# Performance work log

Measured on AMD Instinct MI355X. Metric: run time of the kernel, lower is better.

## Reference

```python
import jax, jax.numpy as jnp
import numpy as np

T, N, D, E = 4, 50000, 32, 800000
V_TH = 1.0      # v_threshold
ALPHA = 4.0     # surrogate-gradient sharpness


def setup_inputs() -> dict:
    key = jax.random.key(0)
    k1, k2, k3, k4 = jax.random.split(key, 4)
    s_seq = jax.random.normal(k1, (T, N, D), dtype=jnp.float32) * 0.5
    z_seq = jax.random.normal(k2, (N, D), dtype=jnp.float32) * 0.5
    edge_index = jax.random.randint(k3, (2, E), 0, N, dtype=jnp.int64)
    # GCNConv weight (bias=False), Glorot-ish scale
    W = jax.random.normal(k4, (D, D), dtype=jnp.float32) / np.sqrt(D).astype(np.float32)
    return {"s_seq": s_seq, "z_seq": z_seq, "W": W, "edge_index": edge_index}


def _gcn_conv(x, W, edge_index, n_nodes):
    """PyG GCNConv with add_self_loops=True, normalize=True, bias=False.
    x: [T,N,D]; returns [T,N,D]."""
    src, dst = edge_index[0], edge_index[1]
    ones = jnp.ones(src.shape[0], dtype=x.dtype)
    deg = jax.ops.segment_sum(ones, dst, num_segments=n_nodes) + 1.0  # +1 self loop
    dinv = jax.lax.rsqrt(deg)                                        # [N]
    xw = jnp.einsum('tnd,df->tnf', x, W)                             # dense transform
    norm = dinv[src] * dinv[dst]                                     # [E]
    msgs = xw[:, src, :] * norm[None, :, None]                       # [T,E,D] gather
    agg = jax.vmap(lambda m: jax.ops.segment_sum(m, dst, num_segments=n_nodes))(msgs)
    # self-loop contribution with norm dinv[i]^2
    return agg + xw * (dinv * dinv)[None, :, None]


def _spike(v):
    # Heaviside spike with surrogate (sigmoid) gradient, straight-through.
    s = (v >= V_TH).astype(v.dtype)
    sg = jax.nn.sigmoid(ALPHA * (v - V_TH))
    return s + sg - jax.lax.stop_gradient(sg)


def reference(s_seq, z_seq, W, edge_index):
    n_nodes = s_seq.shape[1]
    x_seq = _gcn_conv(s_seq, W, edge_index, n_nodes)   # [T,N,D]  (dropout p=0.0 is identity)
    y_seq = x_seq.mean(0)                              # temporal mean [N,D]
    # Riemannian IF node: integrate-and-fire over time with soft reset;
    # latent state z drifts by the temporal mean (Euclidean proxy for expmap).
    def step(v, x_t):
        v = v + x_t
        o = _spike(v)
        v = v - o * V_TH
        return v, o
    v0 = jnp.zeros_like(z_seq)
    _, o_seq = jax.lax.scan(step, v0, x_seq)           # [T,N,D]
    z_new = z_seq + y_seq
    return o_seq, z_new
```

## Files before the change

### kernel.cpp

```cpp
#include <hip/hip_runtime.h>
#include <hip/hip_fp16.h>

#define TSTEPS 4
#define DIM 32
#define BINW_SHIFT 8
#define NB 256
#define HB 128
#define GROWS 128
#define SP_CH 2048
#define PAD_PER_BIN 772

__device__ __forceinline__ float4 ldx4h(const __half* p) {
    uint2 u = *(const uint2*)p;
    __half2 h0 = *(__half2*)&u.x;
    __half2 h1 = *(__half2*)&u.y;
    float2 a = __half22float2(h0);
    float2 b = __half22float2(h1);
    return make_float4(a.x, a.y, b.x, b.y);
}

__global__ __launch_bounds__(256) void hist_kernel(
    const int* __restrict__ ei, int* __restrict__ ghistPB, int* __restrict__ cursor,
    int E, int hch) {
    __shared__ int lh[NB];
    int tid = threadIdx.x;
    lh[tid] = 0;
    __syncthreads();
    int beg = blockIdx.x * hch;
    int end = min(beg + hch, E);
    for (int e = beg + tid; e < end; e += 256)
        atomicAdd(&lh[ei[E + e] >> BINW_SHIFT], 1);
    __syncthreads();
    ghistPB[blockIdx.x * NB + tid] = lh[tid];
    if (blockIdx.x == 0) cursor[tid] = 0;
}

__global__ __launch_bounds__(256) void splitgemm_kernel(
    const int* __restrict__ ei, const int* __restrict__ ghistPB,
    int* __restrict__ cursor, unsigned int* __restrict__ esorted,
    int* __restrict__ binScan,
    const float* __restrict__ s, const float* __restrict__ W,
    __half* __restrict__ xwp, int E, int rows, int N, int nchunks) {
    __shared__ __align__(16) char smem[22528];
    int tid = threadIdx.x;

    if ((int)blockIdx.x >= nchunks) {
        float4 (*sW4)[8] = (float4 (*)[8])smem;
        float  (*sS)[36] = (float (*)[36])(smem + 4096);
        int row = tid >> 3;
        int cg  = tid & 7;
        sW4[row][cg] = ((const float4*)W)[tid];
        int rowBase = ((int)blockIdx.x - nchunks) * GROWS;
#pragma unroll
        for (int j = 0; j < 4; j++) {
            int r = rowBase + row + j * 32;
            float4 sv = (r < rows) ? ((const float4*)s)[(size_t)r * 8 + cg]
                                   : make_float4(0.f, 0.f, 0.f, 0.f);
            *(float4*)&sS[row + j * 32][cg * 4] = sv;
        }
        __syncthreads();
        float4 a0 = make_float4(0.f, 0.f, 0.f, 0.f);
        float4 a1 = a0, a2 = a0, a3 = a0;
#pragma unroll
        for (int k = 0; k < 32; k++) {
            float4 wv = sW4[k][cg];
            float s0 = sS[row][k];
            float s1 = sS[row + 32][k];
            float s2 = sS[row + 64][k];
            float s3 = sS[row + 96][k];
            a0.x += s0 * wv.x; a0.y += s0 * wv.y; a0.z += s0 * wv.z; a0.w += s0 * wv.w;
            a1.x += s1 * wv.x; a1.y += s1 * wv.y; a1.z += s1 * wv.z; a1.w += s1 * wv.w;
            a2.x += s2 * wv.x; a2.y += s2 * wv.y; a2.z += s2 * wv.z; a2.w += s2 * wv.w;
            a3.x += s3 * wv.x; a3.y += s3 * wv.y; a3.z += s3 * wv.z; a3.w += s3 * wv.w;
        }
        float4 accs[4] = {a0, a1, a2, a3};
#pragma unroll
        for (int j = 0; j < 4; j++) {
            int r = rowBase + row + j * 32;
            if (r < rows) {
                int t = r / N;
                int n = r - t * N;
                __half2 h0 = __floats2half2_rn(accs[j].x, accs[j].y);
                __half2 h1 = __floats2half2_rn(accs[j].z, accs[j].w);
                uint2 u;
                u.x = *(unsigned int*)&h0;
                u.y = *(unsigned int*)&h1;
                *(uint2*)(xwp + (size_t)n * 128 + t * 32 + cg * 4) = u;
            }
        }
        return;
    }

    int* phw   = (int*)smem;
    int* sBS   = (int*)(smem + 4096);
    int* pscan = (int*)(smem + 5120);
    int* gb    = (int*)(smem + 6144);
    int* pcur  = (int*)(smem + 7168);
    unsigned int* sbuf = (unsigned int*)(smem + 8192);

    int gv = 0;
    for (int r = 0; r < HB; r++) gv += ghistPB[r * NB + tid];
    sBS[tid] = gv;
    __syncthreads();
    for (int off = 1; off < 256; off <<= 1) {
        int t = (tid >= off) ? sBS[tid - off] : 0;
        __syncthreads();
        sBS[tid] += t;
        __syncthreads();
    }
    int binStart = sBS[tid] - gv;
    if (blockIdx.x == 0) binScan[tid] = sBS[tid];
    phw[0 * NB + tid] = 0; phw[1 * NB + tid] = 0;
    phw[2 * NB + tid] = 0; phw[3 * NB + tid] = 0;
    __syncthreads();
    int beg = blockIdx.x * SP_CH;
    int end = min(beg + SP_CH, E);
    int cnt = end - beg;
    int wv = tid >> 6;
    for (int e = beg + tid; e < end; e += 256)
        atomicAdd(&phw[wv * NB + (ei[E + e] >> BINW_SHIFT)], 1);
    __syncthreads();
    int v = phw[0 * NB + tid] + phw[1 * NB + tid] + phw[2 * NB + tid] + phw[3 * NB + tid];
    pscan[tid] = v;
    __syncthreads();
    for (int off = 1; off < 256; off <<= 1) {
        int t = (tid >= off) ? pscan[tid - off] : 0;
        __syncthreads();
        pscan[tid] += t;
        __syncthreads();
    }
    pscan[tid] -= v;
    pcur[tid] = pscan[tid];
    gb[tid] = v ? (binStart + atomicAdd(&cursor[tid], v)) : 0;
    __syncthreads();
    for (int e = beg + tid; e < end; e += 256) {
        int sx = ei[e];
        int dx = ei[E + e];
        unsigned int pk = (unsigned int)sx | ((unsigned int)dx << 16);
        int b = dx >> BINW_SHIFT;
        int p = atomicAdd(&pcur[b], 1);
        sbuf[p] = pk;
    }
    __syncthreads();
    for (int idx = tid; idx < cnt; idx += 256) {
        unsigned int e = sbuf[idx];
        int b = e >> 24;
        esorted[gb[b] + (idx - pscan[b])] = e;
    }
}

__global__ __launch_bounds__(256) void csr_kernel(
    const int* __restrict__ binScan, const unsigned int* __restrict__ esorted,
    int* __restrict__ rec, int* __restrict__ offs, int* __restrict__ deg,
    float* __restrict__ dinv, int N) {
    __shared__ int lh[NB], sc[NB], loff[NB], lcur[NB];
    __shared__ int s_ebeg, s_cnt;
    int bin = blockIdx.x;
    int tid = threadIdx.x;
    if (tid == 0) {
        int e0 = bin ? binScan[bin - 1] : 0;
        int e1 = binScan[bin];
        s_ebeg = e0;
        s_cnt = e1 - e0;
    }
    lh[tid] = 0;
    __syncthreads();
    int ebeg = s_ebeg;
    int cnt = s_cnt;
    int gbase = ((ebeg + 3) & ~3) + PAD_PER_BIN * bin;
    for (int i = tid; i < cnt; i += 256)
        atomicAdd(&lh[(esorted[ebeg + i] >> 16) & 255], 1);
    __syncthreads();
    int padded = (lh[tid] + 3) & ~3;
    sc[tid] = padded;
    __syncthreads();
    for (int off = 1; off < 256; off <<= 1) {
        int t = (tid >= off) ? sc[tid - off] : 0;
        __syncthreads();
        sc[tid] += t;
        __syncthreads();
    }
    loff[tid] = sc[tid] - padded;
    lcur[tid] = 0;
    __syncthreads();
    for (int i = tid; i < cnt; i += 256) {
        unsigned int e = esorted[ebeg + i];
        int ln = (e >> 16) & 255;
        int p = atomicAdd(&lcur[ln], 1);
        rec[gbase + loff[ln] + p] = (int)(e & 0xFFFFu);
    }
    int n = (bin << BINW_SHIFT) + tid;
    if (n < N) {
        offs[n] = gbase + loff[tid];
        deg[n] = lh[tid];
        dinv[n] = rsqrtf((float)lh[tid] + 1.0f);
    }
}

__global__ __launch_bounds__(256) void gather_kernel(
    const int* __restrict__ rec, const int* __restrict__ offs,
    const int* __restrict__ deg, const __half* __restrict__ xwp,
    const float* __restrict__ dinv, const float* __restrict__ z,
    float* __restrict__ out, int N) {
    int gid = blockIdx.x * 256 + threadIdx.x;
    int n = gid >> 5;
    if (n >= N) return;
    int wl = threadIdx.x & 63;
    int half_ = wl >> 5;
    int l = wl & 31;
    int q = l & 7;
    long lofs = l * 4;

    float dn = dinv[n];
    int beg = offs[n];
    int cntn = deg[n];

    float4 acc = make_float4(0.f, 0.f, 0.f, 0.f);
    int i = 0;
    for (; i + 8 <= cntn; i += 8) {
        int4 sa = *(const int4*)(rec + beg + i);
        int4 sb = *(const int4*)(rec + beg + i + 4);
        float n0 = dinv[sa.x] * dn, n1 = dinv[sa.y] * dn;
        float n2 = dinv[sa.z] * dn, n3 = dinv[sa.w] * dn;
        float n4 = dinv[sb.x] * dn, n5 = dinv[sb.y] * dn;
        float n6 = dinv[sb.z] * dn, n7 = dinv[sb.w] * dn;
        float4 p0 = ldx4h(xwp + (long)sa.x * 128 + lofs);
        float4 p1 = ldx4h(xwp + (long)sa.y * 128 + lofs);
        float4 p2 = ldx4h(xwp + (long)sa.z * 128 + lofs);
        float4 p3 = ldx4h(xwp + (long)sa.w * 128 + lofs);
        float4 p4 = ldx4h(xwp + (long)sb.x * 128 + lofs);
        float4 p5 = ldx4h(xwp + (long)sb.y * 128 + lofs);
        float4 p6 = ldx4h(xwp + (long)sb.z * 128 + lofs);
        float4 p7 = ldx4h(xwp + (long)sb.w * 128 + lofs);
        acc.x += n0 * p0.x + n1 * p1.x + n2 * p2.x + n3 * p3.x
               + n4 * p4.x + n5 * p5.x + n6 * p6.x + n7 * p7.x;
        acc.y += n0 * p0.y + n1 * p1.y + n2 * p2.y + n3 * p3.y
               + n4 * p4.y + n5 * p5.y + n6 * p6.y + n7 * p7.y;
        acc.z += n0 * p0.z + n1 * p1.z + n2 * p2.z + n3 * p3.z
               + n4 * p4.z + n5 * p5.z + n6 * p6.z + n7 * p7.z;
        acc.w += n0 * p0.w + n1 * p1.w + n2 * p2.w + n3 * p3.w
               + n4 * p4.w + n5 * p5.w + n6 * p6.w + n7 * p7.w;
    }
    for (; i < cntn; i += 4) {
        int4 s4 = *(const int4*)(rec + beg + i);
        int rem = cntn - i;
        int i0 = s4.x;
        int i1 = (rem > 1) ? s4.y : i0;
        int i2 = (rem > 2) ? s4.z : i0;
        int i3 = (rem > 3) ? s4.w : i0;
        float n0 = dinv[i0] * dn;
        float n1 = (rem > 1) ? dinv[i1] * dn : 0.f;
        float n2 = (rem > 2) ? dinv[i2] * dn : 0.f;
        float n3 = (rem > 3) ? dinv[i3] * dn : 0.f;
        float4 p0 = ldx4h(xwp + (long)i0 * 128 + lofs);
        float4 p1 = ldx4h(xwp + (long)i1 * 128 + lofs);
        float4 p2 = ldx4h(xwp + (long)i2 * 128 + lofs);
        float4 p3 = ldx4h(xwp + (long)i3 * 128 + lofs);
        acc.x += n0 * p0.x + n1 * p1.x + n2 * p2.x + n3 * p3.x;
        acc.y += n0 * p0.y + n1 * p1.y + n2 * p2.y + n3 * p3.y;
        acc.z += n0 * p0.z + n1 * p1.z + n2 * p2.z + n3 * p3.z;
        acc.w += n0 * p0.w + n1 * p1.w + n2 * p2.w + n3 * p3.w;
    }
    {
        float d2 = dn * dn;
        float4 ps = ldx4h(xwp + (long)n * 128 + lofs);
        acc.x += d2 * ps.x;
        acc.y += d2 * ps.y;
        acc.z += d2 * ps.z;
        acc.w += d2 * ps.w;
    }
    float4 xs[TSTEPS];
#pragma unroll
    for (int t = 0; t < TSTEPS; t++) {
        int srcLane = half_ * 32 + t * 8 + q;
        xs[t].x = __shfl(acc.x, srcLane, 64);
        xs[t].y = __shfl(acc.y, srcLane, 64);
        xs[t].z = __shfl(acc.z, srcLane, 64);
        xs[t].w = __shfl(acc.w, srcLane, 64);
    }
    if (l < 8) {
        float4 y;
        y.x = (xs[0].x + xs[1].x + xs[2].x + xs[3].x) * 0.25f;
        y.y = (xs[0].y + xs[1].y + xs[2].y + xs[3].y) * 0.25f;
        y.z = (xs[0].z + xs[1].z + xs[2].z + xs[3].z) * 0.25f;
        y.w = (xs[0].w + xs[1].w + xs[2].w + xs[3].w) * 0.25f;
        float4 v = make_float4(0.f, 0.f, 0.f, 0.f);
        int colBase = n * 32 + q * 4;
#pragma unroll
        for (int t = 0; t < TSTEPS; t++) {
            float4 o;
            v.x += xs[t].x; o.x = (v.x >= 1.0f) ? 1.0f : 0.0f; v.x -= o.x;
            v.y += xs[t].y; o.y = (v.y >= 1.0f) ? 1.0f : 0.0f; v.y -= o.y;
            v.z += xs[t].z; o.z = (v.z >= 1.0f) ? 1.0f : 0.0f; v.z -= o.z;
            v.w += xs[t].w; o.w = (v.w >= 1.0f) ? 1.0f : 0.0f; v.w -= o.w;
            *(float4*)(out + (size_t)t * N * 32 + colBase) = o;
        }
        float4 zv = *(const float4*)(z + colBase);
        float4 zn;
        zn.x = zv.x + y.x;
        zn.y = zv.y + y.y;
        zn.z = zv.z + y.z;
        zn.w = zv.w + y.w;
        *(float4*)(out + (size_t)TSTEPS * N * 32 + colBase) = zn;
    }
}

extern "C" void kernel_launch(void* const* d_in, const int* in_sizes, int n_in,
                              void* d_out, int out_size, void* d_ws, size_t ws_size,
                              hipStream_t stream) {
    const float* s_seq = (const float*)d_in[0];
    const float* z_seq = (const float*)d_in[1];
    const float* W     = (const float*)d_in[2];
    const int*   ei    = (const int*)d_in[3];
    float* out = (float*)d_out;

    int N = in_sizes[1] / DIM;
    int E = in_sizes[3] / 2;
    int rows = TSTEPS * N;
    int nb = (N + 255) >> BINW_SHIFT;
    int nchunks = (E + SP_CH - 1) / SP_CH;

    char* w = (char*)d_ws;
    __half* xwp          = (__half*)w;       w += (size_t)rows * DIM * 2;
    unsigned int* esorted = (unsigned int*)w; w += (size_t)E * 4;
    int*   rec      = (int*)w;    w += ((size_t)E + PAD_PER_BIN * nb + 16) * 4;
    int*   offs     = (int*)w;    w += (size_t)N * 4;
    int*   deg      = (int*)w;    w += (size_t)N * 4;
    float* dinv     = (float*)w;  w += (size_t)N * 4;
    int*   ghistPB  = (int*)w;    w += (size_t)HB * NB * 4;
    int*   cursor   = (int*)w;    w += NB * 4;
    int*   binScan  = (int*)w;    w += NB * 4;

    int hch = (E + HB - 1) / HB;
    int xwBlocks = (rows + GROWS - 1) / GROWS;
    hist_kernel<<<HB, 256, 0, stream>>>(ei, ghistPB, cursor, E, hch);
    splitgemm_kernel<<<nchunks + xwBlocks, 256, 0, stream>>>(
        ei, ghistPB, cursor, esorted, binScan, s_seq, W, xwp, E, rows, N, nchunks);
    csr_kernel<<<nb, 256, 0, stream>>>(binScan, esorted, rec, offs, deg, dinv, N);
    gather_kernel<<<(N * 32 + 255) / 256, 256, 0, stream>>>(rec, offs, deg, xwp,
                                                            dinv, z_seq, out, N);
}
```

Baseline: 181.7 us.

## Replace binned two-pass edge sort with global-atomic degree count and direct CSR scatter

Drops the binned counting-sort pipeline (per-block histograms, bin scan, staged shared-memory sort, per-bin CSR build) and builds the CSR directly. Degrees come from global atomics, per-256-node block offsets come from a scan plus an atomic base, and each edge is scattered into its destination row with a global atomic cursor. The scatter is fused with the XW GEMM in one launch. This removes the esorted intermediate and several scans, at the cost of heavy global atomic contention and uncoalesced scattered writes. Edge order within a row is also now nondeterministic.

```diff
diff --git a/kernel.cpp b/kernel.cpp
--- a/kernel.cpp
+++ b/kernel.cpp
@@ -3,12 +3,8 @@
 
 #define TSTEPS 4
 #define DIM 32
-#define BINW_SHIFT 8
 #define NB 256
-#define HB 128
 #define GROWS 128
-#define SP_CH 2048
-#define PAD_PER_BIN 772
 
 __device__ __forceinline__ float4 ldx4h(const __half* p) {
     uint2 u = *(const uint2*)p;
@@ -19,159 +15,22 @@
     return make_float4(a.x, a.y, b.x, b.y);
 }
 
-__global__ __launch_bounds__(256) void hist_kernel(
-    const int* __restrict__ ei, int* __restrict__ ghistPB, int* __restrict__ cursor,
-    int E, int hch) {
-    __shared__ int lh[NB];
+__global__ __launch_bounds__(256) void deg_kernel(
+    const int* __restrict__ ei, int* __restrict__ deg, int E) {
+    int stride = gridDim.x * 256;
+    for (int e = blockIdx.x * 256 + threadIdx.x; e < E; e += stride)
+        atomicAdd(&deg[ei[E + e]], 1);
+}
+
+__global__ __launch_bounds__(256) void offs_kernel(
+    const int* __restrict__ deg, int* __restrict__ offs,
+    float* __restrict__ dinv, int* __restrict__ cursor0, int N) {
+    __shared__ int sc[NB];
+    __shared__ int s_base;
     int tid = threadIdx.x;
-    lh[tid] = 0;
-    __syncthreads();
-    int beg = blockIdx.x * hch;
-    int end = min(beg + hch, E);
-    for (int e = beg + tid; e < end; e += 256)
-        atomicAdd(&lh[ei[E + e] >> BINW_SHIFT], 1);
-    __syncthreads();
-    ghistPB[blockIdx.x * NB + tid] = lh[tid];
-    if (blockIdx.x == 0) cursor[tid] = 0;
-}
-
-__global__ __launch_bounds__(256) void splitgemm_kernel(
-    const int* __restrict__ ei, const int* __restrict__ ghistPB,
-    int* __restrict__ cursor, unsigned int* __restrict__ esorted,
-    int* __restrict__ binScan,
-    const float* __restrict__ s, const float* __restrict__ W,
-    __half* __restrict__ xwp, int E, int rows, int N, int nchunks) {
-    __shared__ __align__(16) char smem[22528];
-    int tid = threadIdx.x;
-
-    if ((int)blockIdx.x >= nchunks) {
-        float4 (*sW4)[8] = (float4 (*)[8])smem;
-        float  (*sS)[36] = (float (*)[36])(smem + 4096);
-        int row = tid >> 3;
-        int cg  = tid & 7;
-        sW4[row][cg] = ((const float4*)W)[tid];
-        int rowBase = ((int)blockIdx.x - nchunks) * GROWS;
-#pragma unroll
-        for (int j = 0; j < 4; j++) {
-            int r = rowBase + row + j * 32;
-            float4 sv = (r < rows) ? ((const float4*)s)[(size_t)r * 8 + cg]
-                                   : make_float4(0.f, 0.f, 0.f, 0.f);
-            *(float4*)&sS[row + j * 32][cg * 4] = sv;
-        }
-        __syncthreads();
-        float4 a0 = make_float4(0.f, 0.f, 0.f, 0.f);
-        float4 a1 = a0, a2 = a0, a3 = a0;
-#pragma unroll
-        for (int k = 0; k < 32; k++) {
-            float4 wv = sW4[k][cg];
-            float s0 = sS[row][k];
-            float s1 = sS[row + 32][k];
-            float s2 = sS[row + 64][k];
-            float s3 = sS[row + 96][k];
-            a0.x += s0 * wv.x; a0.y += s0 * wv.y; a0.z += s0 * wv.z; a0.w += s0 * wv.w;
-            a1.x += s1 * wv.x; a1.y += s1 * wv.y; a1.z += s1 * wv.z; a1.w += s1 * wv.w;
-            a2.x += s2 * wv.x; a2.y += s2 * wv.y; a2.z += s2 * wv.z; a2.w += s2 * wv.w;
-            a3.x += s3 * wv.x; a3.y += s3 * wv.y; a3.z += s3 * wv.z; a3.w += s3 * wv.w;
-        }
-        float4 accs[4] = {a0, a1, a2, a3};
-#pragma unroll
-        for (int j = 0; j < 4; j++) {
-            int r = rowBase + row + j * 32;
-            if (r < rows) {
-                int t = r / N;
-                int n = r - t * N;
-                __half2 h0 = __floats2half2_rn(accs[j].x, accs[j].y);
-                __half2 h1 = __floats2half2_rn(accs[j].z, accs[j].w);
-                uint2 u;
-                u.x = *(unsigned int*)&h0;
-                u.y = *(unsigned int*)&h1;
-                *(uint2*)(xwp + (size_t)n * 128 + t * 32 + cg * 4) = u;
-            }
-        }
-        return;
-    }
-
-    int* phw   = (int*)smem;
-    int* sBS   = (int*)(smem + 4096);
-    int* pscan = (int*)(smem + 5120);
-    int* gb    = (int*)(smem + 6144);
-    int* pcur  = (int*)(smem + 7168);
-    unsigned int* sbuf = (unsigned int*)(smem + 8192);
-
-    int gv = 0;
-    for (int r = 0; r < HB; r++) gv += ghistPB[r * NB + tid];
-    sBS[tid] = gv;
-    __syncthreads();
-    for (int off = 1; off < 256; off <<= 1) {
-        int t = (tid >= off) ? sBS[tid - off] : 0;
-        __syncthreads();
-        sBS[tid] += t;
-        __syncthreads();
-    }
-    int binStart = sBS[tid] - gv;
-    if (blockIdx.x == 0) binScan[tid] = sBS[tid];
-    phw[0 * NB + tid] = 0; phw[1 * NB + tid] = 0;
-    phw[2 * NB + tid] = 0; phw[3 * NB + tid] = 0;
-    __syncthreads();
-    int beg = blockIdx.x * SP_CH;
-    int end = min(beg + SP_CH, E);
-    int cnt = end - beg;
-    int wv = tid >> 6;
-    for (int e = beg + tid; e < end; e += 256)
-        atomicAdd(&phw[wv * NB + (ei[E + e] >> BINW_SHIFT)], 1);
-    __syncthreads();
-    int v = phw[0 * NB + tid] + phw[1 * NB + tid] + phw[2 * NB + tid] + phw[3 * NB + tid];
-    pscan[tid] = v;
-    __syncthreads();
-    for (int off = 1; off < 256; off <<= 1) {
-        int t = (tid >= off) ? pscan[tid - off] : 0;
-        __syncthreads();
-        pscan[tid] += t;
-        __syncthreads();
-    }
-    pscan[tid] -= v;
-    pcur[tid] = pscan[tid];
-    gb[tid] = v ? (binStart + atomicAdd(&cursor[tid], v)) : 0;
-    __syncthreads();
-    for (int e = beg + tid; e < end; e += 256) {
-        int sx = ei[e];
-        int dx = ei[E + e];
-        unsigned int pk = (unsigned int)sx | ((unsigned int)dx << 16);
-        int b = dx >> BINW_SHIFT;
-        int p = atomicAdd(&pcur[b], 1);
-        sbuf[p] = pk;
-    }
-    __syncthreads();
-    for (int idx = tid; idx < cnt; idx += 256) {
-        unsigned int e = sbuf[idx];
-        int b = e >> 24;
-        esorted[gb[b] + (idx - pscan[b])] = e;
-    }
-}
-
-__global__ __launch_bounds__(256) void csr_kernel(
-    const int* __restrict__ binScan, const unsigned int* __restrict__ esorted,
-    int* __restrict__ rec, int* __restrict__ offs, int* __restrict__ deg,
-    float* __restrict__ dinv, int N) {
-    __shared__ int lh[NB], sc[NB], loff[NB], lcur[NB];
-    __shared__ int s_ebeg, s_cnt;
-    int bin = blockIdx.x;
-    int tid = threadIdx.x;
-    if (tid == 0) {
-        int e0 = bin ? binScan[bin - 1] : 0;
-        int e1 = binScan[bin];
-        s_ebeg = e0;
-        s_cnt = e1 - e0;
-    }
-    lh[tid] = 0;
-    __syncthreads();
-    int ebeg = s_ebeg;
-    int cnt = s_cnt;
-    int gbase = ((ebeg + 3) & ~3) + PAD_PER_BIN * bin;
-    for (int i = tid; i < cnt; i += 256)
-        atomicAdd(&lh[(esorted[ebeg + i] >> 16) & 255], 1);
-    __syncthreads();
-    int padded = (lh[tid] + 3) & ~3;
+    int n = (blockIdx.x << 8) + tid;
+    int d = (n < N) ? deg[n] : 0;
+    int padded = (d + 3) & ~3;
     sc[tid] = padded;
     __syncthreads();
     for (int off = 1; off < 256; off <<= 1) {
@@ -180,20 +39,75 @@
         sc[tid] += t;
         __syncthreads();
     }
-    loff[tid] = sc[tid] - padded;
-    lcur[tid] = 0;
+    if (tid == 255) s_base = atomicAdd(cursor0, sc[255]);
     __syncthreads();
-    for (int i = tid; i < cnt; i += 256) {
-        unsigned int e = esorted[ebeg + i];
-        int ln = (e >> 16) & 255;
-        int p = atomicAdd(&lcur[ln], 1);
-        rec[gbase + loff[ln] + p] = (int)(e & 0xFFFFu);
-    }
-    int n = (bin << BINW_SHIFT) + tid;
     if (n < N) {
-        offs[n] = gbase + loff[tid];
-        deg[n] = lh[tid];
-        dinv[n] = rsqrtf((float)lh[tid] + 1.0f);
+        offs[n] = s_base + sc[tid] - padded;
+        dinv[n] = rsqrtf((float)d + 1.0f);
+    }
+}
+
+__global__ __launch_bounds__(256) void scattergemm_kernel(
+    const int* __restrict__ ei, const int* __restrict__ offs,
+    int* __restrict__ cur, int* __restrict__ rec,
+    const float* __restrict__ s, const float* __restrict__ W,
+    __half* __restrict__ xwp, int E, int rows, int N, int scBlocks) {
+    __shared__ __align__(16) char smem[22528];
+    int tid = threadIdx.x;
+
+    if ((int)blockIdx.x < scBlocks) {
+        int e = blockIdx.x * 256 + tid;
+        if (e < E) {
+            int src = ei[e];
+            int dst = ei[E + e];
+            int p = atomicAdd(&cur[dst], 1);
+            rec[offs[dst] + p] = src;
+        }
+        return;
+    }
+
+    float4 (*sW4)[8] = (float4 (*)[8])smem;
+    float  (*sS)[36] = (float (*)[36])(smem + 4096);
+    int row = tid >> 3;
+    int cg  = tid & 7;
+    sW4[row][cg] = ((const float4*)W)[tid];
+    int rowBase = ((int)blockIdx.x - scBlocks) * GROWS;
+#pragma unroll
+    for (int j = 0; j < 4; j++) {
+        int r = rowBase + row + j * 32;
+        float4 sv = (r < rows) ? ((const float4*)s)[(size_t)r * 8 + cg]
+                               : make_float4(0.f, 0.f, 0.f, 0.f);
+        *(float4*)&sS[row + j * 32][cg * 4] = sv;
+    }
+    __syncthreads();
+    float4 a0 = make_float4(0.f, 0.f, 0.f, 0.f);
+    float4 a1 = a0, a2 = a0, a3 = a0;
+#pragma unroll
+    for (int k = 0; k < 32; k++) {
+        float4 wv = sW4[k][cg];
+        float s0 = sS[row][k];
+        float s1 = sS[row + 32][k];
+        float s2 = sS[row + 64][k];
+        float s3 = sS[row + 96][k];
+        a0.x += s0 * wv.x; a0.y += s0 * wv.y; a0.z += s0 * wv.z; a0.w += s0 * wv.w;
+        a1.x += s1 * wv.x; a1.y += s1 * wv.y; a1.z += s1 * wv.z; a1.w += s1 * wv.w;
+        a2.x += s2 * wv.x; a2.y += s2 * wv.y; a2.z += s2 * wv.z; a2.w += s2 * wv.w;
+        a3.x += s3 * wv.x; a3.y += s3 * wv.y; a3.z += s3 * wv.z; a3.w += s3 * wv.w;
+    }
+    float4 accs[4] = {a0, a1, a2, a3};
+#pragma unroll
+    for (int j = 0; j < 4; j++) {
+        int r = rowBase + row + j * 32;
+        if (r < rows) {
+            int t = r / N;
+            int n = r - t * N;
+            __half2 h0 = __floats2half2_rn(accs[j].x, accs[j].y);
+            __half2 h1 = __floats2half2_rn(accs[j].z, accs[j].w);
+            uint2 u;
+            u.x = *(unsigned int*)&h0;
+            u.y = *(unsigned int*)&h1;
+            *(uint2*)(xwp + (size_t)n * 128 + t * 32 + cg * 4) = u;
+        }
     }
 }
 
@@ -317,26 +231,26 @@
     int N = in_sizes[1] / DIM;
     int E = in_sizes[3] / 2;
     int rows = TSTEPS * N;
-    int nb = (N + 255) >> BINW_SHIFT;
-    int nchunks = (E + SP_CH - 1) / SP_CH;
+    int nbin = (N + 255) >> 8;
 
     char* w = (char*)d_ws;
-    __half* xwp          = (__half*)w;       w += (size_t)rows * DIM * 2;
-    unsigned int* esorted = (unsigned int*)w; w += (size_t)E * 4;
-    int*   rec      = (int*)w;    w += ((size_t)E + PAD_PER_BIN * nb + 16) * 4;
-    int*   offs     = (int*)w;    w += (size_t)N * 4;
-    int*   deg      = (int*)w;    w += (size_t)N * 4;
-    float* dinv     = (float*)w;  w += (size_t)N * 4;
-    int*   ghistPB  = (int*)w;    w += (size_t)HB * NB * 4;
-    int*   cursor   = (int*)w;    w += NB * 4;
-    int*   binScan  = (int*)w;    w += NB * 4;
-
-    int hch = (E + HB - 1) / HB;
+    __half* xwp = (__half*)w;  w += (size_t)rows * DIM * 2;
+    int*   rec  = (int*)w;     w += ((size_t)E + 4 * (size_t)N + 64) * 4;
+    int*   offs = (int*)w;     w += (size_t)N * 4;
+    float* dinv = (float*)w;   w += (size_t)N * 4;
+    int*   deg  = (int*)w;     w += (size_t)N * 4;
+    int*   cur  = (int*)w;     w += (size_t)N * 4;
+    int*   cursor0 = (int*)w;  w += 64;
+
+    hipMemsetAsync(deg, 0, ((size_t)2 * N + 16) * 4, stream);
+
+    int scBlocks = (E + 255) / 256;
     int xwBlocks = (rows + GROWS - 1) / GROWS;
-    hist_kernel<<<HB, 256, 0, stream>>>(ei, ghistPB, cursor, E, hch);
-    splitgemm_kernel<<<nchunks + xwBlocks, 256, 0, stream>>>(
-        ei, ghistPB, cursor, esorted, binScan, s_seq, W, xwp, E, rows, N, nchunks);
-    csr_kernel<<<nb, 256, 0, stream>>>(binScan, esorted, rec, offs, deg, dinv, N);
+
+    deg_kernel<<<512, 256, 0, stream>>>(ei, deg, E);
+    offs_kernel<<<nbin, 256, 0, stream>>>(deg, offs, dinv, cursor0, N);
+    scattergemm_kernel<<<scBlocks + xwBlocks, 256, 0, stream>>>(
+        ei, offs, cur, rec, s_seq, W, xwp, E, rows, N, scBlocks);
     gather_kernel<<<(N * 32 + 255) / 256, 256, 0, stream>>>(rec, offs, deg, xwp,
                                                             dinv, z_seq, out, N);
 }
```

Measured after the change: 222.3 us. 22.3% more time.

## Replace atomic-cursor bin scatter with deterministic per-chunk histogram column scan

Applied to the files above, without the earlier changes.

The coarse bin sort is restructured. Per-chunk histograms are now computed alongside the dense transform in one kernel. A new column-scan kernel derives each chunk's exclusive offset per bin, and the split kernel then places edges at deterministic positions without a global atomic cursor. Each split block no longer reads 128 partial histograms or recounts its chunk, and the csr kernel rescans bin totals itself. The cost is one extra kernel launch, plus a 512-thread scan that caps the chunk count at 512.

```diff
diff --git a/kernel.cpp b/kernel.cpp
--- a/kernel.cpp
+++ b/kernel.cpp
@@ -5,7 +5,6 @@
 #define DIM 32
 #define BINW_SHIFT 8
 #define NB 256
-#define HB 128
 #define GROWS 128
 #define SP_CH 2048
 #define PAD_PER_BIN 772
@@ -19,120 +18,126 @@
     return make_float4(a.x, a.y, b.x, b.y);
 }
 
-__global__ __launch_bounds__(256) void hist_kernel(
-    const int* __restrict__ ei, int* __restrict__ ghistPB, int* __restrict__ cursor,
-    int E, int hch) {
-    __shared__ int lh[NB];
-    int tid = threadIdx.x;
-    lh[tid] = 0;
-    __syncthreads();
-    int beg = blockIdx.x * hch;
-    int end = min(beg + hch, E);
-    for (int e = beg + tid; e < end; e += 256)
-        atomicAdd(&lh[ei[E + e] >> BINW_SHIFT], 1);
-    __syncthreads();
-    ghistPB[blockIdx.x * NB + tid] = lh[tid];
-    if (blockIdx.x == 0) cursor[tid] = 0;
-}
-
-__global__ __launch_bounds__(256) void splitgemm_kernel(
-    const int* __restrict__ ei, const int* __restrict__ ghistPB,
-    int* __restrict__ cursor, unsigned int* __restrict__ esorted,
-    int* __restrict__ binScan,
+__global__ __launch_bounds__(256) void histgemm_kernel(
+    const int* __restrict__ ei, int* __restrict__ ghist,
     const float* __restrict__ s, const float* __restrict__ W,
     __half* __restrict__ xwp, int E, int rows, int N, int nchunks) {
     __shared__ __align__(16) char smem[22528];
     int tid = threadIdx.x;
 
-    if ((int)blockIdx.x >= nchunks) {
-        float4 (*sW4)[8] = (float4 (*)[8])smem;
-        float  (*sS)[36] = (float (*)[36])(smem + 4096);
-        int row = tid >> 3;
-        int cg  = tid & 7;
-        sW4[row][cg] = ((const float4*)W)[tid];
-        int rowBase = ((int)blockIdx.x - nchunks) * GROWS;
-#pragma unroll
-        for (int j = 0; j < 4; j++) {
-            int r = rowBase + row + j * 32;
-            float4 sv = (r < rows) ? ((const float4*)s)[(size_t)r * 8 + cg]
-                                   : make_float4(0.f, 0.f, 0.f, 0.f);
-            *(float4*)&sS[row + j * 32][cg * 4] = sv;
+    if ((int)blockIdx.x < nchunks) {
+        int* lh = (int*)smem;
+        lh[tid] = 0;
+        __syncthreads();
+        int beg = blockIdx.x * SP_CH;
+        int end = min(beg + SP_CH, E);
+        for (int e = beg + tid; e < end; e += 256)
+            atomicAdd(&lh[ei[E + e] >> BINW_SHIFT], 1);
+        __syncthreads();
+        ghist[(size_t)blockIdx.x * NB + tid] = lh[tid];
+        return;
+    }
+
+    float4 (*sW4)[8] = (float4 (*)[8])smem;
+    float  (*sS)[36] = (float (*)[36])(smem + 4096);
+    int row = tid >> 3;
+    int cg  = tid & 7;
+    sW4[row][cg] = ((const float4*)W)[tid];
+    int rowBase = ((int)blockIdx.x - nchunks) * GROWS;
+#pragma unroll
+    for (int j = 0; j < 4; j++) {
+        int r = rowBase + row + j * 32;
+        float4 sv = (r < rows) ? ((const float4*)s)[(size_t)r * 8 + cg]
+                               : make_float4(0.f, 0.f, 0.f, 0.f);
+        *(float4*)&sS[row + j * 32][cg * 4] = sv;
+    }
+    __syncthreads();
+    float4 a0 = make_float4(0.f, 0.f, 0.f, 0.f);
+    float4 a1 = a0, a2 = a0, a3 = a0;
+#pragma unroll
+    for (int k = 0; k < 32; k++) {
+        float4 wv = sW4[k][cg];
+        float s0 = sS[row][k];
+        float s1 = sS[row + 32][k];
+        float s2 = sS[row + 64][k];
+        float s3 = sS[row + 96][k];
+        a0.x += s0 * wv.x; a0.y += s0 * wv.y; a0.z += s0 * wv.z; a0.w += s0 * wv.w;
+        a1.x += s1 * wv.x; a1.y += s1 * wv.y; a1.z += s1 * wv.z; a1.w += s1 * wv.w;
+        a2.x += s2 * wv.x; a2.y += s2 * wv.y; a2.z += s2 * wv.z; a2.w += s2 * wv.w;
+        a3.x += s3 * wv.x; a3.y += s3 * wv.y; a3.z += s3 * wv.z; a3.w += s3 * wv.w;
+    }
+    float4 accs[4] = {a0, a1, a2, a3};
+#pragma unroll
+    for (int j = 0; j < 4; j++) {
+        int r = rowBase + row + j * 32;
+        if (r < rows) {
+            int t = r / N;
+            int n = r - t * N;
+            __half2 h0 = __floats2half2_rn(accs[j].x, accs[j].y);
+            __half2 h1 = __floats2half2_rn(accs[j].z, accs[j].w);
+            uint2 u;
+            u.x = *(unsigned int*)&h0;
+            u.y = *(unsigned int*)&h1;
+            *(uint2*)(xwp + (size_t)n * 128 + t * 32 + cg * 4) = u;
         }
-        __syncthreads();
-        float4 a0 = make_float4(0.f, 0.f, 0.f, 0.f);
-        float4 a1 = a0, a2 = a0, a3 = a0;
-#pragma unroll
-        for (int k = 0; k < 32; k++) {
-            float4 wv = sW4[k][cg];
-            float s0 = sS[row][k];
-            float s1 = sS[row + 32][k];
-            float s2 = sS[row + 64][k];
-            float s3 = sS[row + 96][k];
-            a0.x += s0 * wv.x; a0.y += s0 * wv.y; a0.z += s0 * wv.z; a0.w += s0 * wv.w;
-            a1.x += s1 * wv.x; a1.y += s1 * wv.y; a1.z += s1 * wv.z; a1.w += s1 * wv.w;
-            a2.x += s2 * wv.x; a2.y += s2 * wv.y; a2.z += s2 * wv.z; a2.w += s2 * wv.w;
-            a3.x += s3 * wv.x; a3.y += s3 * wv.y; a3.z += s3 * wv.z; a3.w += s3 * wv.w;
-        }
-        float4 accs[4] = {a0, a1, a2, a3};
-#pragma unroll
-        for (int j = 0; j < 4; j++) {
-            int r = rowBase + row + j * 32;
-            if (r < rows) {
-                int t = r / N;
-                int n = r - t * N;
-                __half2 h0 = __floats2half2_rn(accs[j].x, accs[j].y);
-                __half2 h1 = __floats2half2_rn(accs[j].z, accs[j].w);
-                uint2 u;
-                u.x = *(unsigned int*)&h0;
-                u.y = *(unsigned int*)&h1;
-                *(uint2*)(xwp + (size_t)n * 128 + t * 32 + cg * 4) = u;
-            }
-        }
-        return;
-    }
-
-    int* phw   = (int*)smem;
-    int* sBS   = (int*)(smem + 4096);
-    int* pscan = (int*)(smem + 5120);
-    int* gb    = (int*)(smem + 6144);
-    int* pcur  = (int*)(smem + 7168);
-    unsigned int* sbuf = (unsigned int*)(smem + 8192);
-
-    int gv = 0;
-    for (int r = 0; r < HB; r++) gv += ghistPB[r * NB + tid];
-    sBS[tid] = gv;
+    }
+}
+
+__global__ __launch_bounds__(512) void colscan_kernel(
+    const int* __restrict__ ghist, int* __restrict__ ghist2,
+    int* __restrict__ totals, int nchunks) {
+    __shared__ int sc[512];
+    int t = threadIdx.x;
+    int b = blockIdx.x;
+    int v = (t < nchunks) ? ghist[(size_t)t * NB + b] : 0;
+    sc[t] = v;
+    __syncthreads();
+    for (int off = 1; off < 512; off <<= 1) {
+        int tv = (t >= off) ? sc[t - off] : 0;
+        __syncthreads();
+        sc[t] += tv;
+        __syncthreads();
+    }
+    if (t < nchunks) ghist2[(size_t)t * NB + b] = sc[t] - v;
+    if (t == 511) totals[b] = sc[511];
+}
+
+__global__ __launch_bounds__(256) void split_kernel(
+    const int* __restrict__ ei, const int* __restrict__ ghist,
+    const int* __restrict__ ghist2, const int* __restrict__ totals,
+    unsigned int* __restrict__ esorted, int E) {
+    __shared__ int binB[NB], pscan[NB], gb[NB], pcur[NB];
+    __shared__ unsigned int sbuf[SP_CH];
+    int tid = threadIdx.x;
+    int bid = blockIdx.x;
+
+    int tot = totals[tid];
+    binB[tid] = tot;
     __syncthreads();
     for (int off = 1; off < 256; off <<= 1) {
-        int t = (tid >= off) ? sBS[tid - off] : 0;
-        __syncthreads();
-        sBS[tid] += t;
-        __syncthreads();
-    }
-    int binStart = sBS[tid] - gv;
-    if (blockIdx.x == 0) binScan[tid] = sBS[tid];
-    phw[0 * NB + tid] = 0; phw[1 * NB + tid] = 0;
-    phw[2 * NB + tid] = 0; phw[3 * NB + tid] = 0;
-    __syncthreads();
-    int beg = blockIdx.x * SP_CH;
+        int t = (tid >= off) ? binB[tid - off] : 0;
+        __syncthreads();
+        binB[tid] += t;
+        __syncthreads();
+    }
+    int v = ghist[(size_t)bid * NB + tid];
+    pscan[tid] = v;
+    __syncthreads();
+    for (int off = 1; off < 256; off <<= 1) {
+        int t = (tid >= off) ? pscan[tid - off] : 0;
+        __syncthreads();
+        pscan[tid] += t;
+        __syncthreads();
+    }
+    int pexcl = pscan[tid] - v;
+    pscan[tid] = pexcl;
+    pcur[tid] = pexcl;
+    gb[tid] = (binB[tid] - tot) + ghist2[(size_t)bid * NB + tid] - pexcl;
+    __syncthreads();
+
+    int beg = bid * SP_CH;
     int end = min(beg + SP_CH, E);
     int cnt = end - beg;
-    int wv = tid >> 6;
-    for (int e = beg + tid; e < end; e += 256)
-        atomicAdd(&phw[wv * NB + (ei[E + e] >> BINW_SHIFT)], 1);
-    __syncthreads();
-    int v = phw[0 * NB + tid] + phw[1 * NB + tid] + phw[2 * NB + tid] + phw[3 * NB + tid];
-    pscan[tid] = v;
-    __syncthreads();
-    for (int off = 1; off < 256; off <<= 1) {
-        int t = (tid >= off) ? pscan[tid - off] : 0;
-        __syncthreads();
-        pscan[tid] += t;
-        __syncthreads();
-    }
-    pscan[tid] -= v;
-    pcur[tid] = pscan[tid];
-    gb[tid] = v ? (binStart + atomicAdd(&cursor[tid], v)) : 0;
-    __syncthreads();
     for (int e = beg + tid; e < end; e += 256) {
         int sx = ei[e];
         int dx = ei[E + e];
@@ -145,25 +150,32 @@
     for (int idx = tid; idx < cnt; idx += 256) {
         unsigned int e = sbuf[idx];
         int b = e >> 24;
-        esorted[gb[b] + (idx - pscan[b])] = e;
+        esorted[gb[b] + idx] = e;
     }
 }
 
 __global__ __launch_bounds__(256) void csr_kernel(
-    const int* __restrict__ binScan, const unsigned int* __restrict__ esorted,
+    const int* __restrict__ totals, const unsigned int* __restrict__ esorted,
     int* __restrict__ rec, int* __restrict__ offs, int* __restrict__ deg,
     float* __restrict__ dinv, int N) {
     __shared__ int lh[NB], sc[NB], loff[NB], lcur[NB];
     __shared__ int s_ebeg, s_cnt;
     int bin = blockIdx.x;
     int tid = threadIdx.x;
+    sc[tid] = totals[tid];
+    lh[tid] = 0;
+    __syncthreads();
+    for (int off = 1; off < 256; off <<= 1) {
+        int t = (tid >= off) ? sc[tid - off] : 0;
+        __syncthreads();
+        sc[tid] += t;
+        __syncthreads();
+    }
     if (tid == 0) {
-        int e0 = bin ? binScan[bin - 1] : 0;
-        int e1 = binScan[bin];
+        int e0 = bin ? sc[bin - 1] : 0;
         s_ebeg = e0;
-        s_cnt = e1 - e0;
-    }
-    lh[tid] = 0;
+        s_cnt = sc[bin] - e0;
+    }
     __syncthreads();
     int ebeg = s_ebeg;
     int cnt = s_cnt;
@@ -321,22 +333,22 @@
     int nchunks = (E + SP_CH - 1) / SP_CH;
 
     char* w = (char*)d_ws;
-    __half* xwp          = (__half*)w;       w += (size_t)rows * DIM * 2;
+    __half* xwp           = (__half*)w;       w += (size_t)rows * DIM * 2;
     unsigned int* esorted = (unsigned int*)w; w += (size_t)E * 4;
-    int*   rec      = (int*)w;    w += ((size_t)E + PAD_PER_BIN * nb + 16) * 4;
-    int*   offs     = (int*)w;    w += (size_t)N * 4;
-    int*   deg      = (int*)w;    w += (size_t)N * 4;
-    float* dinv     = (float*)w;  w += (size_t)N * 4;
-    int*   ghistPB  = (int*)w;    w += (size_t)HB * NB * 4;
-    int*   cursor   = (int*)w;    w += NB * 4;
-    int*   binScan  = (int*)w;    w += NB * 4;
-
-    int hch = (E + HB - 1) / HB;
+    int*   rec    = (int*)w;  w += ((size_t)E + PAD_PER_BIN * nb + 16) * 4;
+    int*   offs   = (int*)w;  w += (size_t)N * 4;
+    int*   deg    = (int*)w;  w += (size_t)N * 4;
+    float* dinv   = (float*)w; w += (size_t)N * 4;
+    int*   ghist  = (int*)w;  w += (size_t)nchunks * NB * 4;
+    int*   ghist2 = (int*)w;  w += (size_t)nchunks * NB * 4;
+    int*   totals = (int*)w;  w += NB * 4;
+
     int xwBlocks = (rows + GROWS - 1) / GROWS;
-    hist_kernel<<<HB, 256, 0, stream>>>(ei, ghistPB, cursor, E, hch);
-    splitgemm_kernel<<<nchunks + xwBlocks, 256, 0, stream>>>(
-        ei, ghistPB, cursor, esorted, binScan, s_seq, W, xwp, E, rows, N, nchunks);
-    csr_kernel<<<nb, 256, 0, stream>>>(binScan, esorted, rec, offs, deg, dinv, N);
+    histgemm_kernel<<<nchunks + xwBlocks, 256, 0, stream>>>(
+        ei, ghist, s_seq, W, xwp, E, rows, N, nchunks);
+    colscan_kernel<<<NB, 512, 0, stream>>>(ghist, ghist2, totals, nchunks);
+    split_kernel<<<nchunks, 256, 0, stream>>>(ei, ghist, ghist2, totals, esorted, E);
+    csr_kernel<<<nb, 256, 0, stream>>>(totals, esorted, rec, offs, deg, dinv, N);
     gather_kernel<<<(N * 32 + 255) / 256, 256, 0, stream>>>(rec, offs, deg, xwp,
                                                             dinv, z_seq, out, N);
 }
```

Result: faster. 170.2 us (-6.3%).
